# Kernel optimization log

Measured on AMD Instinct MI355X. Metric: run time of the kernel, lower is better.

The kernel has to match this reference:

```python
import jax, jax.numpy as jnp
import numpy as np

QUERY_DIM = 256
HIDDEN_DIM = 256
NUM_HEADS = 8
HEAD_DIM = HIDDEN_DIM // NUM_HEADS
NORM_FACT = float(HIDDEN_DIM / NUM_HEADS) ** (-0.5)


def setup_inputs() -> dict:
    key = jax.random.key(0)
    ks = jax.random.split(key, 7)
    b, Q, H, W = 4, 300, 100, 100
    q = jax.random.normal(ks[0], (b, Q, QUERY_DIM), dtype=jnp.float32)
    k = jax.random.normal(ks[1], (b, QUERY_DIM, H, W), dtype=jnp.float32)
    mask = jax.random.randint(ks[2], (b, H, W), 0, 2).astype(jnp.bool_)
    # xavier_uniform for Linear(query_dim, hidden_dim): bound = sqrt(6/(fan_in+fan_out))
    bound = float(np.sqrt(6.0 / (QUERY_DIM + HIDDEN_DIM)))
    q_w = jax.random.uniform(ks[3], (HIDDEN_DIM, QUERY_DIM), jnp.float32, -bound, bound)
    k_w = jax.random.uniform(ks[4], (HIDDEN_DIM, QUERY_DIM), jnp.float32, -bound, bound)
    q_b = jnp.zeros((HIDDEN_DIM,), jnp.float32)
    k_b = jnp.zeros((HIDDEN_DIM,), jnp.float32)
    return {"q": q, "k": k, "mask": mask, "q_w": q_w, "q_b": q_b, "k_w": k_w, "k_b": k_b}


def reference(q, k, mask, q_w, q_b, k_w, k_b):
    b, Q, _ = q.shape
    _, C, H, W = k.shape
    # q_linear: [b,Q,query_dim] -> [b,Q,hidden]
    qp = jnp.einsum('bqc,hc->bqh', q, q_w) + q_b
    # k projection: 1x1 conv == channel-wise linear: [b,C,H,W] -> [b,hidden,H,W]
    kp = jnp.einsum('bchw,oc->bohw', k, k_w) + k_b[None, :, None, None]
    qh = qp.reshape(b, Q, NUM_HEADS, HEAD_DIM)
    kh = kp.reshape(b, NUM_HEADS, HEAD_DIM, H, W)
    # attention scores: [b, Q, n_heads, H, W]
    weights = jnp.einsum('bqnc,bnchw->bqnhw', qh * NORM_FACT, kh)
    if mask is not None:
        weights = jnp.where(mask[:, None, None, :, :], -jnp.inf, weights)
    # softmax over flattened (heads, H, W) — faithful to flatten(2) in the original
    flat = weights.reshape(b, Q, NUM_HEADS * H * W)
    weights = jax.nn.softmax(flat, axis=-1).reshape(b, Q, NUM_HEADS, H, W)
    return weights
```

## Files before the change

kernel.cpp:

```cpp
#include <hip/hip_runtime.h>
#include <math.h>

#define BB 4
#define QQ 300
#define CC 256
#define NH 8
#define HD 32
#define HWN 10000
#define NT 625
#define NCHUNK 125
#define TPC 5
#define MT 19
#define NORM_FACT 0.17677669529663687f

typedef __attribute__((ext_vector_type(8))) short short8_t;
typedef __attribute__((ext_vector_type(4))) float f32x4_t;
typedef __attribute__((ext_vector_type(4))) int   i32x4_t;

union FragU { uint32_t u[4]; short8_t v; };

__device__ __forceinline__ unsigned short bf16_rn(float x) {
    uint32_t u = __float_as_uint(x);
    return (unsigned short)((u + 0x7fffu + ((u >> 16) & 1u)) >> 16);
}
__device__ __forceinline__ float bf16_f(unsigned short h) {
    return __uint_as_float(((uint32_t)h) << 16);
}

__global__ void prep_kwB_kernel(const float* __restrict__ kw,
                                unsigned short* __restrict__ kwB_hi,
                                unsigned short* __restrict__ kwB_lo) {
    const int ot = blockIdx.x, ks = blockIdx.y;
    const int l = threadIdx.x;
    const int o = ot * 16 + (l & 15);
    const int c0 = ks * 32 + (l >> 4) * 8;
    const size_t base = ((size_t)(ot * 8 + ks) * 64 + l) * 8;
    #pragma unroll
    for (int j = 0; j < 8; ++j) {
        const float x = kw[o * CC + c0 + j];
        const unsigned short h = bf16_rn(x);
        kwB_hi[base + j] = h;
        kwB_lo[base + j] = bf16_rn(x - bf16_f(h));
    }
}

__global__ __launch_bounds__(256)
void qproj_kernel(const float* __restrict__ qin,
                  const unsigned short* __restrict__ qwB_hi,
                  const unsigned short* __restrict__ qwB_lo,
                  const float* __restrict__ qb,
                  unsigned short* __restrict__ qp_il) {
    const int wid = threadIdx.x >> 6, l = threadIdx.x & 63;
    const int rt = blockIdx.x;
    const int ot4 = wid;
    const int jb = (l >> 4) * 8;
    const int col = l & 15;

    FragU a_hi[8], a_lo[8];
    const float* abase = qin + ((size_t)rt * 16 + col) * CC;
    #pragma unroll
    for (int ks = 0; ks < 8; ++ks) {
        #pragma unroll
        for (int tt = 0; tt < 4; ++tt) {
            const int c = ks * 32 + jb + 2 * tt;
            const float x0 = abase[c];
            const float x1 = abase[c + 1];
            const unsigned short h0 = bf16_rn(x0), h1 = bf16_rn(x1);
            const unsigned short g0 = bf16_rn(x0 - bf16_f(h0));
            const unsigned short g1 = bf16_rn(x1 - bf16_f(h1));
            a_hi[ks].u[tt] = (uint32_t)h0 | ((uint32_t)h1 << 16);
            a_lo[ks].u[tt] = (uint32_t)g0 | ((uint32_t)g1 << 16);
        }
    }

    #pragma unroll 1
    for (int t = 0; t < 4; ++t) {
        const int ot = ot4 * 4 + t;
        f32x4_t c = {0.f, 0.f, 0.f, 0.f};
        #pragma unroll
        for (int ks = 0; ks < 8; ++ks) {
            const size_t fb = ((size_t)(ot * 8 + ks) * 64 + l) * 8;
            const short8_t bh = *reinterpret_cast<const short8_t*>(qwB_hi + fb);
            const short8_t bl = *reinterpret_cast<const short8_t*>(qwB_lo + fb);
            c = __builtin_amdgcn_mfma_f32_16x16x32_bf16(a_hi[ks].v, bh, c, 0, 0, 0);
            c = __builtin_amdgcn_mfma_f32_16x16x32_bf16(a_hi[ks].v, bl, c, 0, 0, 0);
            c = __builtin_amdgcn_mfma_f32_16x16x32_bf16(a_lo[ks].v, bh, c, 0, 0, 0);
        }
        const int o = ot * 16 + col;
        const int n = o >> 5, osub = o & 31;
        const float bias = qb[o];
        #pragma unroll
        for (int r = 0; r < 4; ++r) {
            const int row = rt * 16 + (l >> 4) * 4 + r;
            const float v = (c[r] + bias) * NORM_FACT;
            const size_t base = ((size_t)row * NH + n) * 64 + osub;
            const unsigned short h = bf16_rn(v);
            qp_il[base]      = h;
            qp_il[base + 32] = bf16_rn(v - bf16_f(h));
        }
    }
}

__global__ __launch_bounds__(256)
void kproj_kernel(const float* __restrict__ kin,
                  const unsigned short* __restrict__ kwB_hi,
                  const unsigned short* __restrict__ kwB_lo,
                  const float* __restrict__ kb,
                  unsigned short* __restrict__ kp_il) {
    __shared__ float kf[CC][17];
    const int wid = threadIdx.x >> 6, l = threadIdx.x & 63;
    const int bu  = blockIdx.x;
    const int hwt = bu % NT;
    const int b   = bu / NT;
    const int ot4 = wid;

    {
        const int tid = threadIdx.x;
        const float* kb0 = kin + (size_t)b * CC * HWN + hwt * 16;
        #pragma unroll
        for (int iter = 0; iter < 4; ++iter) {
            const int c   = iter * 64 + (tid >> 2);
            const int cl  = (tid & 3) * 4;
            const float4 v = *reinterpret_cast<const float4*>(
                kb0 + (size_t)c * HWN + cl);
            kf[c][cl]     = v.x;
            kf[c][cl + 1] = v.y;
            kf[c][cl + 2] = v.z;
            kf[c][cl + 3] = v.w;
        }
    }
    __syncthreads();

    const int jb  = (l >> 4) * 8;
    const int col = l & 15;

    f32x4_t acc[4];
    #pragma unroll
    for (int t = 0; t < 4; ++t) {
        const float bias = kb[(ot4 * 4 + t) * 16 + col];
        acc[t] = {bias, bias, bias, bias};
    }

    #pragma unroll 2
    for (int ks = 0; ks < 8; ++ks) {
        FragU a_hi, a_lo;
        #pragma unroll
        for (int tt = 0; tt < 4; ++tt) {
            const int c = ks * 32 + jb + 2 * tt;
            const float x0 = kf[c][col];
            const float x1 = kf[c + 1][col];
            const unsigned short h0 = bf16_rn(x0), h1 = bf16_rn(x1);
            const unsigned short g0 = bf16_rn(x0 - bf16_f(h0));
            const unsigned short g1 = bf16_rn(x1 - bf16_f(h1));
            a_hi.u[tt] = (uint32_t)h0 | ((uint32_t)h1 << 16);
            a_lo.u[tt] = (uint32_t)g0 | ((uint32_t)g1 << 16);
        }
        #pragma unroll
        for (int t = 0; t < 4; ++t) {
            const int ot = ot4 * 4 + t;
            const size_t fb = ((size_t)(ot * 8 + ks) * 64 + l) * 8;
            const short8_t bh = *reinterpret_cast<const short8_t*>(kwB_hi + fb);
            const short8_t bl = *reinterpret_cast<const short8_t*>(kwB_lo + fb);
            acc[t] = __builtin_amdgcn_mfma_f32_16x16x32_bf16(a_hi.v, bh, acc[t], 0, 0, 0);
            acc[t] = __builtin_amdgcn_mfma_f32_16x16x32_bf16(a_hi.v, bl, acc[t], 0, 0, 0);
            acc[t] = __builtin_amdgcn_mfma_f32_16x16x32_bf16(a_lo.v, bh, acc[t], 0, 0, 0);
        }
    }

    #pragma unroll
    for (int t = 0; t < 4; ++t) {
        const int o = (ot4 * 4 + t) * 16 + col;
        const int n = o >> 5, osub = o & 31;
        #pragma unroll
        for (int r = 0; r < 4; ++r) {
            const int hwrow = hwt * 16 + (l >> 4) * 4 + r;
            const size_t base = ((size_t)(b * HWN + hwrow) * NH + n) * 64 + osub;
            const float v = acc[t][r];
            const unsigned short h = bf16_rn(v);
            kp_il[base]      = h;
            kp_il[base + 32] = bf16_rn(v - bf16_f(h));
        }
    }
}

__global__ __launch_bounds__(256)
void attn_stats_kernel(const unsigned short* __restrict__ qp_il,
                       const unsigned short* __restrict__ kp_il,
                       const int* __restrict__ mask,
                       float* __restrict__ partials) {
    const int wid = threadIdx.x >> 6, l = threadIdx.x & 63;
    const int wu = blockIdx.x * 4 + wid;
    const int qh = wu & 1;
    int tmp = wu >> 1;
    const int ch = tmp % NCHUNK; tmp /= NCHUNK;
    const int n = tmp & 7;
    const int b = tmp >> 3;

    short8_t ah[TPC], al[TPC];
    float mf[TPC][4];
    #pragma unroll
    for (int t = 0; t < TPC; ++t) {
        const int tile = ch * TPC + t;
        const int hwr = tile * 16 + (l & 15);
        const size_t abase = ((size_t)(b * HWN + hwr) * NH + n) * 64 + (l >> 4) * 8;
        ah[t] = *reinterpret_cast<const short8_t*>(kp_il + abase);
        al[t] = *reinterpret_cast<const short8_t*>(kp_il + abase + 32);
        const int hw4 = tile * 16 + (l >> 4) * 4;
        const i32x4_t mv = *reinterpret_cast<const i32x4_t*>(mask + b * HWN + hw4);
        mf[t][0] = mv.x ? 0.f : 1.f;
        mf[t][1] = mv.y ? 0.f : 1.f;
        mf[t][2] = mv.z ? 0.f : 1.f;
        mf[t][3] = mv.w ? 0.f : 1.f;
    }

    const int qt0 = qh * 10;
    const int qt1 = qh ? MT : 10;
    #pragma unroll 2
    for (int qt = qt0; qt < qt1; ++qt) {
        const int qa = qt * 16 + (l & 15);
        const int qcl = qa < QQ ? qa : QQ - 1;
        const size_t bbase = ((size_t)(b * QQ + qcl) * NH + n) * 64 + (l >> 4) * 8;
        const short8_t bh = *reinterpret_cast<const short8_t*>(qp_il + bbase);
        const short8_t bl = *reinterpret_cast<const short8_t*>(qp_il + bbase + 32);

        float a = 0.f;
        #pragma unroll
        for (int t = 0; t < TPC; ++t) {
            f32x4_t c = {0.f, 0.f, 0.f, 0.f};
            c = __builtin_amdgcn_mfma_f32_16x16x32_bf16(ah[t], bh, c, 0, 0, 0);
            c = __builtin_amdgcn_mfma_f32_16x16x32_bf16(ah[t], bl, c, 0, 0, 0);
            c = __builtin_amdgcn_mfma_f32_16x16x32_bf16(al[t], bh, c, 0, 0, 0);
            a += __expf(c[0]) * mf[t][0] + __expf(c[1]) * mf[t][1]
               + __expf(c[2]) * mf[t][2] + __expf(c[3]) * mf[t][3];
        }
        a += __shfl_xor(a, 16, 64);
        a += __shfl_xor(a, 32, 64);
        if (l < 16) {
            const int qr = qt * 16 + l;
            if (qr < QQ)
                partials[(((size_t)b * QQ + qr) * NH + n) * NCHUNK + ch] = a;
        }
    }
}

__global__ void invsum_kernel(const float* __restrict__ partials,
                              float* __restrict__ invS) {
    const int row = blockIdx.x;
    const int l = threadIdx.x;
    float s = 0.f;
    const float* p = partials + (size_t)row * (NH * NCHUNK);
    for (int i = l; i < NH * NCHUNK; i += 64) s += p[i];
    #pragma unroll
    for (int m = 1; m < 64; m <<= 1) s += __shfl_xor(s, m, 64);
    if (l == 0) invS[row] = 1.0f / s;
}

__global__ __launch_bounds__(256)
void attn_out_kernel(const unsigned short* __restrict__ qp_il,
                     const unsigned short* __restrict__ kp_il,
                     const int* __restrict__ mask,
                     const float* __restrict__ invS,
                     float* __restrict__ out) {
    const int wid = threadIdx.x >> 6, l = threadIdx.x & 63;
    const int wu = blockIdx.x * 4 + wid;
    const int qh = wu & 1;
    int tmp = wu >> 1;
    const int ch = tmp % NCHUNK; tmp /= NCHUNK;
    const int n = tmp & 7;
    const int b = tmp >> 3;

    short8_t ah[TPC], al[TPC];
    float mf[TPC][4];
    int hw4v[TPC];
    #pragma unroll
    for (int t = 0; t < TPC; ++t) {
        const int tile = ch * TPC + t;
        const int hwr = tile * 16 + (l & 15);
        const size_t abase = ((size_t)(b * HWN + hwr) * NH + n) * 64 + (l >> 4) * 8;
        ah[t] = *reinterpret_cast<const short8_t*>(kp_il + abase);
        al[t] = *reinterpret_cast<const short8_t*>(kp_il + abase + 32);
        const int hw4 = tile * 16 + (l >> 4) * 4;
        hw4v[t] = hw4;
        const i32x4_t mv = *reinterpret_cast<const i32x4_t*>(mask + b * HWN + hw4);
        mf[t][0] = mv.x ? 0.f : 1.f;
        mf[t][1] = mv.y ? 0.f : 1.f;
        mf[t][2] = mv.z ? 0.f : 1.f;
        mf[t][3] = mv.w ? 0.f : 1.f;
    }

    const int qt0 = qh * 10;
    const int qt1 = qh ? MT : 10;
    #pragma unroll 2
    for (int qt = qt0; qt < qt1; ++qt) {
        const int qa = qt * 16 + (l & 15);
        const int qcl = qa < QQ ? qa : QQ - 1;
        const bool qok = qa < QQ;
        const size_t bbase = ((size_t)(b * QQ + qcl) * NH + n) * 64 + (l >> 4) * 8;
        const short8_t bh = *reinterpret_cast<const short8_t*>(qp_il + bbase);
        const short8_t bl = *reinterpret_cast<const short8_t*>(qp_il + bbase + 32);
        const float is = invS[b * QQ + qcl];
        float* const obase = out + (((size_t)b * QQ + qcl) * NH + n) * HWN;

        #pragma unroll
        for (int t = 0; t < TPC; ++t) {
            f32x4_t c = {0.f, 0.f, 0.f, 0.f};
            c = __builtin_amdgcn_mfma_f32_16x16x32_bf16(ah[t], bh, c, 0, 0, 0);
            c = __builtin_amdgcn_mfma_f32_16x16x32_bf16(ah[t], bl, c, 0, 0, 0);
            c = __builtin_amdgcn_mfma_f32_16x16x32_bf16(al[t], bh, c, 0, 0, 0);
            f32x4_t rv;
            rv[0] = __expf(c[0]) * is * mf[t][0];
            rv[1] = __expf(c[1]) * is * mf[t][1];
            rv[2] = __expf(c[2]) * is * mf[t][2];
            rv[3] = __expf(c[3]) * is * mf[t][3];
            if (qok)
                *reinterpret_cast<f32x4_t*>(obase + hw4v[t]) = rv;
        }
    }
}

extern "C" void kernel_launch(void* const* d_in, const int* in_sizes, int n_in,
                              void* d_out, int out_size, void* d_ws, size_t ws_size,
                              hipStream_t stream) {
    const float* q    = (const float*)d_in[0];
    const float* k    = (const float*)d_in[1];
    const int*   mask = (const int*)d_in[2];
    const float* qw   = (const float*)d_in[3];
    const float* qb   = (const float*)d_in[4];
    const float* kw   = (const float*)d_in[5];
    const float* kb   = (const float*)d_in[6];
    float* out = (float*)d_out;

    char* wsb = (char*)d_ws;
    unsigned short* kp_il = (unsigned short*)wsb;
    unsigned short* qp_il = (unsigned short*)(wsb + 40960000);
    float* invS           = (float*)(wsb + 40960000 + 1228800);

    unsigned short* kwB_hi = (unsigned short*)d_out;
    unsigned short* kwB_lo = kwB_hi + 65536;
    unsigned short* qwB_hi = kwB_hi + 131072;
    unsigned short* qwB_lo = kwB_hi + 196608;
    float* partials = (float*)((char*)d_out + (4u << 20));

    prep_kwB_kernel<<<dim3(16, 8), 64, 0, stream>>>(kw, kwB_hi, kwB_lo);
    prep_kwB_kernel<<<dim3(16, 8), 64, 0, stream>>>(qw, qwB_hi, qwB_lo);
    qproj_kernel<<<75, 256, 0, stream>>>(q, qwB_hi, qwB_lo, qb, qp_il);
    kproj_kernel<<<BB * NT, 256, 0, stream>>>(k, kwB_hi, kwB_lo, kb, kp_il);
    attn_stats_kernel<<<(BB * NH * NCHUNK * 2) / 4, 256, 0, stream>>>(
        qp_il, kp_il, mask, partials);
    invsum_kernel<<<BB * QQ, 64, 0, stream>>>(partials, invS);
    attn_out_kernel<<<(BB * NH * NCHUNK * 2) / 4, 256, 0, stream>>>(
        qp_il, kp_il, mask, invS, out);
}
```

Measured before the change: 224.3 us.

## Restructure attn_out to hold query tiles in registers and use nontemporal stores

The output kernel now splits work into four query chunks of five 16-row tiles and keeps those query fragments, inverse sums and output pointers in registers, while streaming key tiles in the outer loop. Each wave now writes five adjacent 16-column pieces across five query rows instead of many query rows for a fixed column chunk, which changes the store access pattern. Output stores become nontemporal, which keeps the large write-once output from polluting cache. The grid doubles in wave count, each wave doing less work, which may improve load balance but adds repeated key loads.

Result: faster. 219.3 us, median of 2 (-2.2%).

```diff
diff --git a/kernel.cpp b/kernel.cpp
--- a/kernel.cpp
+++ b/kernel.cpp
@@ -10,6 +10,8 @@
 #define NT 625
 #define NCHUNK 125
 #define TPC 5
+#define QCH 4
+#define NQT 5
 #define MT 19
 #define NORM_FACT 0.17677669529663687f
 
@@ -263,57 +265,54 @@
                      float* __restrict__ out) {
     const int wid = threadIdx.x >> 6, l = threadIdx.x & 63;
     const int wu = blockIdx.x * 4 + wid;
-    const int qh = wu & 1;
-    int tmp = wu >> 1;
-    const int ch = tmp % NCHUNK; tmp /= NCHUNK;
+    const int ch = wu % NCHUNK;
+    int tmp = wu / NCHUNK;
+    const int qc = tmp % QCH; tmp /= QCH;
     const int n = tmp & 7;
     const int b = tmp >> 3;
 
-    short8_t ah[TPC], al[TPC];
-    float mf[TPC][4];
-    int hw4v[TPC];
+    short8_t bh[NQT], bl[NQT];
+    float isv[NQT];
+    float* optr[NQT];
+    bool qok[NQT];
+    #pragma unroll
+    for (int tt = 0; tt < NQT; ++tt) {
+        const int qa = (qc * NQT + tt) * 16 + (l & 15);
+        const int qcl = qa < QQ ? qa : QQ - 1;
+        qok[tt] = qa < QQ;
+        const size_t bbase = ((size_t)(b * QQ + qcl) * NH + n) * 64 + (l >> 4) * 8;
+        bh[tt] = *reinterpret_cast<const short8_t*>(qp_il + bbase);
+        bl[tt] = *reinterpret_cast<const short8_t*>(qp_il + bbase + 32);
+        isv[tt] = invS[b * QQ + qcl];
+        optr[tt] = out + (((size_t)b * QQ + qcl) * NH + n) * HWN;
+    }
+
     #pragma unroll
     for (int t = 0; t < TPC; ++t) {
         const int tile = ch * TPC + t;
         const int hwr = tile * 16 + (l & 15);
         const size_t abase = ((size_t)(b * HWN + hwr) * NH + n) * 64 + (l >> 4) * 8;
-        ah[t] = *reinterpret_cast<const short8_t*>(kp_il + abase);
-        al[t] = *reinterpret_cast<const short8_t*>(kp_il + abase + 32);
+        const short8_t ah = *reinterpret_cast<const short8_t*>(kp_il + abase);
+        const short8_t al = *reinterpret_cast<const short8_t*>(kp_il + abase + 32);
         const int hw4 = tile * 16 + (l >> 4) * 4;
-        hw4v[t] = hw4;
         const i32x4_t mv = *reinterpret_cast<const i32x4_t*>(mask + b * HWN + hw4);
-        mf[t][0] = mv.x ? 0.f : 1.f;
-        mf[t][1] = mv.y ? 0.f : 1.f;
-        mf[t][2] = mv.z ? 0.f : 1.f;
-        mf[t][3] = mv.w ? 0.f : 1.f;
-    }
-
-    const int qt0 = qh * 10;
-    const int qt1 = qh ? MT : 10;
-    #pragma unroll 2
-    for (int qt = qt0; qt < qt1; ++qt) {
-        const int qa = qt * 16 + (l & 15);
-        const int qcl = qa < QQ ? qa : QQ - 1;
-        const bool qok = qa < QQ;
-        const size_t bbase = ((size_t)(b * QQ + qcl) * NH + n) * 64 + (l >> 4) * 8;
-        const short8_t bh = *reinterpret_cast<const short8_t*>(qp_il + bbase);
-        const short8_t bl = *reinterpret_cast<const short8_t*>(qp_il + bbase + 32);
-        const float is = invS[b * QQ + qcl];
-        float* const obase = out + (((size_t)b * QQ + qcl) * NH + n) * HWN;
-
-        #pragma unroll
-        for (int t = 0; t < TPC; ++t) {
+        const float m0 = mv.x ? 0.f : 1.f, m1 = mv.y ? 0.f : 1.f;
+        const float m2 = mv.z ? 0.f : 1.f, m3 = mv.w ? 0.f : 1.f;
+        #pragma unroll
+        for (int tt = 0; tt < NQT; ++tt) {
             f32x4_t c = {0.f, 0.f, 0.f, 0.f};
-            c = __builtin_amdgcn_mfma_f32_16x16x32_bf16(ah[t], bh, c, 0, 0, 0);
-            c = __builtin_amdgcn_mfma_f32_16x16x32_bf16(ah[t], bl, c, 0, 0, 0);
-            c = __builtin_amdgcn_mfma_f32_16x16x32_bf16(al[t], bh, c, 0, 0, 0);
+            c = __builtin_amdgcn_mfma_f32_16x16x32_bf16(ah, bh[tt], c, 0, 0, 0);
+            c = __builtin_amdgcn_mfma_f32_16x16x32_bf16(ah, bl[tt], c, 0, 0, 0);
+            c = __builtin_amdgcn_mfma_f32_16x16x32_bf16(al, bh[tt], c, 0, 0, 0);
+            const float is = isv[tt];
             f32x4_t rv;
-            rv[0] = __expf(c[0]) * is * mf[t][0];
-            rv[1] = __expf(c[1]) * is * mf[t][1];
-            rv[2] = __expf(c[2]) * is * mf[t][2];
-            rv[3] = __expf(c[3]) * is * mf[t][3];
-            if (qok)
-                *reinterpret_cast<f32x4_t*>(obase + hw4v[t]) = rv;
+            rv[0] = __expf(c[0]) * is * m0;
+            rv[1] = __expf(c[1]) * is * m1;
+            rv[2] = __expf(c[2]) * is * m2;
+            rv[3] = __expf(c[3]) * is * m3;
+            if (qok[tt])
+                __builtin_nontemporal_store(rv,
+                    reinterpret_cast<f32x4_t*>(optr[tt] + hw4));
         }
     }
 }
@@ -348,6 +347,6 @@
     attn_stats_kernel<<<(BB * NH * NCHUNK * 2) / 4, 256, 0, stream>>>(
         qp_il, kp_il, mask, partials);
     invsum_kernel<<<BB * QQ, 64, 0, stream>>>(partials, invS);
-    attn_out_kernel<<<(BB * NH * NCHUNK * 2) / 4, 256, 0, stream>>>(
+    attn_out_kernel<<<(BB * NH * QCH * NCHUNK) / 4, 256, 0, stream>>>(
         qp_il, kp_il, mask, invS, out);
 }
```
